# Performance work log

Measured on AMD Instinct MI355X. Metric: run time of the kernel, lower is better.

The kernel has to match this reference:

```python
import jax, jax.numpy as jnp
import numpy as np

B, S, E = 8, 4096, 512
QKV, H = 512, 8
D = QKV // H  # head_dim = 64
EPS = 1e-6


def setup_inputs() -> dict:
    key = jax.random.key(0)
    ks = jax.random.split(key, 9)
    sc_in = 1.0 / np.sqrt(E)
    sc_qkv = 1.0 / np.sqrt(QKV)
    # Linear weights stored as [in, out] so y = x @ W + b (equivalent to torch x @ W_t.T + b)
    return {
        "x": jax.random.normal(ks[0], (B, S, E), dtype=jnp.float32),
        "Wq": jax.random.uniform(ks[1], (E, QKV), jnp.float32, -sc_in, sc_in),
        "bq": jax.random.uniform(ks[2], (QKV,), jnp.float32, -sc_in, sc_in),
        "Wk": jax.random.uniform(ks[3], (E, QKV), jnp.float32, -sc_in, sc_in),
        "bk": jax.random.uniform(ks[4], (QKV,), jnp.float32, -sc_in, sc_in),
        "Wv": jax.random.uniform(ks[5], (E, QKV), jnp.float32, -sc_in, sc_in),
        "bv": jax.random.uniform(ks[6], (QKV,), jnp.float32, -sc_in, sc_in),
        "Wo": jax.random.uniform(ks[7], (QKV, E), jnp.float32, -sc_qkv, sc_qkv),
        "bo": jax.random.uniform(ks[8], (E,), jnp.float32, -sc_qkv, sc_qkv),
    }


def feature_map(t):
    # elu(x) + 1 (always positive features)
    return jax.nn.elu(t) + 1.0


def reference(x, Wq, bq, Wk, bk, Wv, bv, Wo, bo):
    bs, seqlen, _ = x.shape
    q = (x @ Wq + bq).reshape(bs, seqlen, H, D)
    k = (x @ Wk + bk).reshape(bs, seqlen, H, D)
    v = (x @ Wv + bv).reshape(bs, seqlen, H, D)
    q = feature_map(q)
    k = feature_map(k)
    # kv: [n, h, m, d] -- per-head outer-product accumulation over sequence
    kv = jnp.einsum('nshd,nshm->nhmd', k, v)
    # normalizer z: [n, l, h]
    z = 1.0 / (jnp.einsum('nlhd,nhd->nlh', q, k.sum(axis=1)) + EPS)
    out = jnp.einsum('nlhd,nhmd,nlh->nlhm', q, kv, z)
    out = out.reshape(bs, seqlen, QKV)
    return out @ Wo + bo
```

## Files before the change

kernel.cpp:

```cpp
#include <hip/hip_runtime.h>
#include <hip/hip_bf16.h>


typedef __bf16 bf16x8 __attribute__((ext_vector_type(8)));
typedef float  f32x4  __attribute__((ext_vector_type(4)));

__device__ __forceinline__ float b2f(unsigned short u) {
    unsigned int x = ((unsigned int)u) << 16;
    return __builtin_bit_cast(float, x);
}
__device__ __forceinline__ unsigned short f2b(float f) {
    unsigned int u = __builtin_bit_cast(unsigned int, f);
    unsigned int r = (u + 0x7FFFu + ((u >> 16) & 1u)) >> 16;
    return (unsigned short)r;
}
__device__ __forceinline__ void load_lds16(const unsigned short* g, unsigned short* l) {
    __builtin_amdgcn_global_load_lds(
        (const __attribute__((address_space(1))) void*)g,
        (__attribute__((address_space(3))) void*)l, 16, 0, 0);
}

__global__ void prep_kernel(const float* __restrict__ x,
                            const float* __restrict__ w0, const float* __restrict__ w1,
                            const float* __restrict__ w2, const float* __restrict__ w3,
                            unsigned short* __restrict__ xb, unsigned short* __restrict__ wt,
                            float* __restrict__ ksg) {
    __shared__ float tile[64][65];
    int t = threadIdx.x;
    if (blockIdx.x >= 256) {
        int i = (blockIdx.x - 256) * 256 + t;
        float4 v = ((const float4*)x)[i];
        ushort4 o;
        o.x = f2b(v.x); o.y = f2b(v.y); o.z = f2b(v.z); o.w = f2b(v.w);
        ((ushort4*)xb)[i] = o;
        return;
    }
    int idx = blockIdx.x;
    if (idx < 16) ksg[idx * 256 + t] = 0.f;
    int bz = idx >> 6, by = (idx >> 3) & 7, bx = idx & 7;
    const float* src = (bz == 0) ? w0 : (bz == 1) ? w1 : (bz == 2) ? w2 : w3;
    unsigned short* dst = wt + (size_t)bz * 512 * 512;
    int rb = by * 64, cb = bx * 64;
    #pragma unroll
    for (int i = 0; i < 16; i++) {
        int c = t + i * 256; int r = c >> 6, cc = c & 63;
        tile[r][cc] = src[(rb + r) * 512 + cb + cc];
    }
    __syncthreads();
    #pragma unroll
    for (int i = 0; i < 16; i++) {
        int c = t + i * 256; int r = c >> 6, cc = c & 63;
        dst[(cb + r) * 512 + rb + cc] = f2b(tile[cc][r]);
    }
}

__global__ __launch_bounds__(256, 4) void gemm_qkv_kernel(
        const unsigned short* __restrict__ xb, const unsigned short* __restrict__ wt,
        const float* __restrict__ bq, const float* __restrict__ bk, const float* __restrict__ bv,
        unsigned short* __restrict__ qb, unsigned short* __restrict__ kT,
        unsigned short* __restrict__ vT, float* __restrict__ ksg) {
    int g = blockIdx.x;
    int xcd = g & 7, slot = g >> 3;
    int mtile = xcd * 32 + slot / 12;
    int tn = slot % 12;
    int tensor = tn >> 2, ntile = tn & 3;
    const unsigned short* Bt = wt + (size_t)tensor * 512 * 512;
    const float* bias = tensor == 0 ? bq : tensor == 1 ? bk : bv;
    bool act = tensor < 2;

    __shared__ __align__(16) unsigned short sA[128 * 64];
    __shared__ __align__(16) unsigned short sB[128 * 64];
    const int tid  = threadIdx.x;
    const int wave = tid >> 6, lane = tid & 63;
    const int wm = wave >> 1, wn = wave & 1;
    const int quad = lane >> 4, l16 = lane & 15;
    const int mbase = mtile * 128, nbase = ntile * 128;
    const int rsub = lane >> 3;
    const int coff = (((lane & 7) ^ rsub) << 3);

    f32x4 acc[4][4];
    #pragma unroll
    for (int i = 0; i < 4; i++)
        #pragma unroll
        for (int j = 0; j < 4; j++) acc[i][j] = (f32x4){0.f, 0.f, 0.f, 0.f};

    for (int kb = 0; kb < 512; kb += 64) {
        #pragma unroll
        for (int t = 0; t < 4; t++) {
            int r0 = t * 32 + wave * 8;
            load_lds16(&xb[(size_t)(mbase + r0 + rsub) * 512 + kb + coff], &sA[r0 * 64]);
            load_lds16(&Bt[(size_t)(nbase + r0 + rsub) * 512 + kb + coff], &sB[r0 * 64]);
        }
        __syncthreads();
        #pragma unroll
        for (int ko = 0; ko < 64; ko += 32) {
            bf16x8 af[4], bfr[4];
            int pg = ((quad + (ko >> 3)) ^ (l16 & 7)) << 3;
            #pragma unroll
            for (int f = 0; f < 4; f++)
                af[f] = *(const bf16x8*)&sA[(wm * 64 + f * 16 + l16) * 64 + pg];
            #pragma unroll
            for (int f = 0; f < 4; f++)
                bfr[f] = *(const bf16x8*)&sB[(wn * 64 + f * 16 + l16) * 64 + pg];
            #pragma unroll
            for (int i = 0; i < 4; i++)
                #pragma unroll
                for (int j = 0; j < 4; j++)
                    acc[i][j] = __builtin_amdgcn_mfma_f32_16x16x32_bf16(af[i], bfr[j], acc[i][j], 0, 0, 0);
        }
        __syncthreads();
    }
    if (tensor == 0) {
        #pragma unroll
        for (int i = 0; i < 4; i++)
            #pragma unroll
            for (int j = 0; j < 4; j++) {
                int gcol = nbase + wn * 64 + j * 16 + l16;
                float bv = bias[gcol];
                #pragma unroll
                for (int r = 0; r < 4; r++) {
                    int grow = mbase + wm * 64 + i * 16 + quad * 4 + r;
                    float v = acc[i][j][r] + bv;
                    v = v > 0.f ? v + 1.f : __expf(v);
                    qb[(size_t)grow * 512 + gcol] = f2b(v);
                }
            }
    } else {
        unsigned short* T = (tensor == 1) ? kT : vT;
        float csum[4] = {0.f, 0.f, 0.f, 0.f};
        #pragma unroll
        for (int i = 0; i < 4; i++)
            #pragma unroll
            for (int j = 0; j < 4; j++) {
                int gcol = nbase + wn * 64 + j * 16 + l16;
                int h = gcol >> 6, d = gcol & 63;
                float bv = bias[gcol];
                int grow0 = mbase + wm * 64 + i * 16 + quad * 4;
                int b = grow0 >> 12, s0 = grow0 & 4095;
                ushort4 o;
                #pragma unroll
                for (int r = 0; r < 4; r++) {
                    float v = acc[i][j][r] + bv;
                    if (act) { v = v > 0.f ? v + 1.f : __expf(v); csum[j] += v; }
                    ((unsigned short*)&o)[r] = f2b(v);
                }
                *(ushort4*)&T[(((size_t)b * 8 + h) * 64 + d) * 4096 + s0] = o;
            }
        if (act) {
            int b = mbase >> 12;
            #pragma unroll
            for (int j = 0; j < 4; j++) {
                float s = csum[j];
                s += __shfl_xor(s, 16, 64);
                s += __shfl_xor(s, 32, 64);
                if (quad == 0) {
                    int gcol = nbase + wn * 64 + j * 16 + l16;
                    atomicAdd(&ksg[b * 512 + gcol], s);
                }
            }
        }
    }
}

__global__ __launch_bounds__(256, 4) void kv_kernel(
        const unsigned short* __restrict__ kT, const unsigned short* __restrict__ vT,
        float* __restrict__ kvp) {
    int bh = blockIdx.x >> 4, sc = blockIdx.x & 15;
    const int tid = threadIdx.x;
    const int wave = tid >> 6, lane = tid & 63;
    const int wm = wave >> 1, wn = wave & 1;
    const int quad = lane >> 4, l16 = lane & 15;
    const int rsub = lane >> 3;
    const int coff = (((lane & 7) ^ rsub) << 3);
    __shared__ __align__(16) unsigned short sV[64 * 64];
    __shared__ __align__(16) unsigned short sK[64 * 64];

    f32x4 acc[2][2];
    #pragma unroll
    for (int i = 0; i < 2; i++)
        #pragma unroll
        for (int j = 0; j < 2; j++) acc[i][j] = (f32x4){0.f, 0.f, 0.f, 0.f};
    size_t base = (size_t)bh * 64 * 4096 + sc * 256;

    for (int kb = 0; kb < 4; kb++) {
        int s0 = kb * 64;
        #pragma unroll
        for (int t = 0; t < 2; t++) {
            int r0 = t * 32 + wave * 8;
            load_lds16(&vT[base + (size_t)(r0 + rsub) * 4096 + s0 + coff], &sV[r0 * 64]);
            load_lds16(&kT[base + (size_t)(r0 + rsub) * 4096 + s0 + coff], &sK[r0 * 64]);
        }
        __syncthreads();
        #pragma unroll
        for (int ko = 0; ko < 64; ko += 32) {
            bf16x8 af[2], bfr[2];
            int pg = ((quad + (ko >> 3)) ^ (l16 & 7)) << 3;
            #pragma unroll
            for (int f = 0; f < 2; f++)
                af[f] = *(const bf16x8*)&sV[(wm * 32 + f * 16 + l16) * 64 + pg];
            #pragma unroll
            for (int f = 0; f < 2; f++)
                bfr[f] = *(const bf16x8*)&sK[(wn * 32 + f * 16 + l16) * 64 + pg];
            #pragma unroll
            for (int i = 0; i < 2; i++)
                #pragma unroll
                for (int j = 0; j < 2; j++)
                    acc[i][j] = __builtin_amdgcn_mfma_f32_16x16x32_bf16(af[i], bfr[j], acc[i][j], 0, 0, 0);
        }
        __syncthreads();
    }
    float* kvout = kvp + ((size_t)sc * 64 + bh) * 4096;
    #pragma unroll
    for (int i = 0; i < 2; i++)
        #pragma unroll
        for (int j = 0; j < 2; j++)
            #pragma unroll
            for (int r = 0; r < 4; r++) {
                int m = wm * 32 + i * 16 + quad * 4 + r;
                int d = wn * 32 + j * 16 + l16;
                kvout[m * 64 + d] = acc[i][j][r];
            }
}

__global__ __launch_bounds__(256) void mid_kernel(
        const float* __restrict__ kvp, unsigned short* __restrict__ kvb) {
    int bh = blockIdx.x >> 2, part = blockIdx.x & 3;
    int tid = threadIdx.x;
    int idx = (part * 256 + tid) * 4;
    float s0 = 0.f, s1 = 0.f, s2 = 0.f, s3 = 0.f;
    #pragma unroll
    for (int sc = 0; sc < 16; sc++) {
        float4 v = *(const float4*)&kvp[((size_t)sc * 64 + bh) * 4096 + idx];
        s0 += v.x; s1 += v.y; s2 += v.z; s3 += v.w;
    }
    ushort4 o; o.x = f2b(s0); o.y = f2b(s1); o.z = f2b(s2); o.w = f2b(s3);
    *(ushort4*)&kvb[(size_t)bh * 4096 + idx] = o;
}

__global__ __launch_bounds__(256, 2) void fused_out_kernel(
        const unsigned short* __restrict__ qb,
        const unsigned short* __restrict__ kvb, const float* __restrict__ ksg,
        const unsigned short* __restrict__ wto, const float* __restrict__ bo,
        float* __restrict__ out) {
    int g = blockIdx.x;
    int xcd = g & 7, slot = g >> 3;
    int mtile = xcd * 32 + (slot >> 2);
    int ntile = slot & 3;

    __shared__ __align__(16) unsigned short sQ[128 * 64];
    __shared__ __align__(16) unsigned short sWo[128 * 64];
    __shared__ __align__(16) unsigned short sKV[64 * 64];
    __shared__ __align__(16) unsigned short sO1[128 * 64];
    __shared__ float sKsum[512];
    __shared__ float sZ[128];
    const int tid  = threadIdx.x;
    const int wave = tid >> 6, lane = tid & 63;
    const int wm = wave >> 1, wn = wave & 1;
    const int quad = lane >> 4, l16 = lane & 15;
    const int mbase = mtile * 128, nbase = ntile * 128;
    const int b = mtile >> 5;
    const int rsub = lane >> 3;
    const int coff = (((lane & 7) ^ rsub) << 3);

    sKsum[tid]       = ksg[b * 512 + tid];
    sKsum[tid + 256] = ksg[b * 512 + 256 + tid];

    f32x4 accm[4][4];
    #pragma unroll
    for (int i = 0; i < 4; i++)
        #pragma unroll
        for (int j = 0; j < 4; j++) accm[i][j] = (f32x4){0.f, 0.f, 0.f, 0.f};

    for (int h = 0; h < 8; h++) {
        #pragma unroll
        for (int t = 0; t < 4; t++) {
            int r0 = t * 32 + wave * 8;
            load_lds16(&qb[(size_t)(mbase + r0 + rsub) * 512 + h * 64 + coff], &sQ[r0 * 64]);
            load_lds16(&wto[(size_t)(nbase + r0 + rsub) * 512 + h * 64 + coff], &sWo[r0 * 64]);
        }
        #pragma unroll
        for (int t = 0; t < 2; t++) {
            int r0 = t * 32 + wave * 8;
            load_lds16(&kvb[(size_t)(b * 8 + h) * 4096 + (r0 + rsub) * 64 + coff], &sKV[r0 * 64]);
        }
        __syncthreads();
        {
            int row = tid >> 1, half = tid & 1;
            const float* ksh = &sKsum[h * 64];
            float dsum = 0.f;
            #pragma unroll
            for (int g2 = 0; g2 < 4; g2++) {
                int G = half * 4 + g2;
                uint4 w = *(const uint4*)&sQ[row * 64 + ((G ^ (row & 7)) << 3)];
                const unsigned int* qp = (const unsigned int*)&w;
                #pragma unroll
                for (int u = 0; u < 4; u++) {
                    int c = G * 8 + u * 2;
                    dsum += __builtin_bit_cast(float, qp[u] << 16)        * ksh[c];
                    dsum += __builtin_bit_cast(float, qp[u] & 0xFFFF0000u) * ksh[c + 1];
                }
            }
            dsum += __shfl_xor(dsum, 1, 64);
            if (!half) sZ[row] = 1.f / (dsum + 1e-6f);
        }
        __syncthreads();
        f32x4 acco[4][2];
        #pragma unroll
        for (int f = 0; f < 4; f++)
            #pragma unroll
            for (int j = 0; j < 2; j++) acco[f][j] = (f32x4){0.f, 0.f, 0.f, 0.f};
        #pragma unroll
        for (int ko = 0; ko < 64; ko += 32) {
            bf16x8 af[4], bfr[2];
            int pg = ((quad + (ko >> 3)) ^ (l16 & 7)) << 3;
            #pragma unroll
            for (int f = 0; f < 4; f++)
                af[f] = *(const bf16x8*)&sQ[(wm * 64 + f * 16 + l16) * 64 + pg];
            #pragma unroll
            for (int j = 0; j < 2; j++)
                bfr[j] = *(const bf16x8*)&sKV[(wn * 32 + j * 16 + l16) * 64 + pg];
            #pragma unroll
            for (int f = 0; f < 4; f++)
                #pragma unroll
                for (int j = 0; j < 2; j++)
                    acco[f][j] = __builtin_amdgcn_mfma_f32_16x16x32_bf16(af[f], bfr[j], acco[f][j], 0, 0, 0);
        }
        #pragma unroll
        for (int f = 0; f < 4; f++)
            #pragma unroll
            for (int j = 0; j < 2; j++)
                #pragma unroll
                for (int r = 0; r < 4; r++) {
                    int row = wm * 64 + f * 16 + quad * 4 + r;
                    int col = wn * 32 + j * 16 + l16;
                    float v = acco[f][j][r] * sZ[row];
                    int grp = col >> 3;
                    sO1[row * 64 + ((grp ^ (row & 7)) << 3) + (col & 7)] = f2b(v);
                }
        __syncthreads();
        #pragma unroll
        for (int ko = 0; ko < 64; ko += 32) {
            bf16x8 af[4], bfr[4];
            int pg = ((quad + (ko >> 3)) ^ (l16 & 7)) << 3;
            #pragma unroll
            for (int f = 0; f < 4; f++)
                af[f] = *(const bf16x8*)&sO1[(wm * 64 + f * 16 + l16) * 64 + pg];
            #pragma unroll
            for (int f = 0; f < 4; f++)
                bfr[f] = *(const bf16x8*)&sWo[(wn * 64 + f * 16 + l16) * 64 + pg];
            #pragma unroll
            for (int i = 0; i < 4; i++)
                #pragma unroll
                for (int j = 0; j < 4; j++)
                    accm[i][j] = __builtin_amdgcn_mfma_f32_16x16x32_bf16(af[i], bfr[j], accm[i][j], 0, 0, 0);
        }
        __syncthreads();
    }
    #pragma unroll
    for (int i = 0; i < 4; i++)
        #pragma unroll
        for (int j = 0; j < 4; j++) {
            int gcol = nbase + wn * 64 + j * 16 + l16;
            float bv = bo[gcol];
            #pragma unroll
            for (int r = 0; r < 4; r++) {
                int grow = mbase + wm * 64 + i * 16 + quad * 4 + r;
                out[(size_t)grow * 512 + gcol] = accm[i][j][r] + bv;
            }
        }
}

extern "C" void kernel_launch(void* const* d_in, const int* in_sizes, int n_in,
                              void* d_out, int out_size, void* d_ws, size_t ws_size,
                              hipStream_t stream) {
    const float* x  = (const float*)d_in[0];
    const float* Wq = (const float*)d_in[1];
    const float* bq = (const float*)d_in[2];
    const float* Wk = (const float*)d_in[3];
    const float* bk = (const float*)d_in[4];
    const float* Wv = (const float*)d_in[5];
    const float* bv = (const float*)d_in[6];
    const float* Wo = (const float*)d_in[7];
    const float* bo = (const float*)d_in[8];
    float* out = (float*)d_out;

    char* wsb = (char*)d_ws;
    char* ob  = (char*)d_out;
    unsigned short* vT  = (unsigned short*)ob;
    unsigned short* xb  = (unsigned short*)(ob + 33554432ull);
    float*          kvp = (float*)(ob + 33554432ull);
    unsigned short* qb  = (unsigned short*)wsb;
    unsigned short* kT  = (unsigned short*)(wsb + 33554432ull);
    unsigned short* wt  = (unsigned short*)(wsb + 67108864ull);
    unsigned short* kvb = (unsigned short*)(wsb + 69206016ull);
    float*          ksg = (float*)(wsb + 69730304ull);

    prep_kernel<<<16640, 256, 0, stream>>>(x, Wq, Wk, Wv, Wo, xb, wt, ksg);
    gemm_qkv_kernel<<<3072, 256, 0, stream>>>(xb, wt, bq, bk, bv, qb, kT, vT, ksg);
    kv_kernel<<<1024, 256, 0, stream>>>(kT, vT, kvp);
    mid_kernel<<<256, 256, 0, stream>>>(kvp, kvb);
    fused_out_kernel<<<1024, 256, 0, stream>>>(qb, kvb, ksg,
            wt + 3ull * 512 * 512, bo, out);
}
```

Before: 259.8 us.

## Widen output tiles to 256 columns and halve kv sequence splits

The fused output kernel now computes a 128x256 output tile per block, two Wo tiles per head. This halves the redundant per-block recomputation of the attention numerator (q·kv and normalizer) and the repeated Q/KV loads. The kv kernel splits the sequence into 8 chunks instead of 16, which halves the partial-sum traffic reduced in mid_kernel. In exchange, doubled accumulators and extra LDS raise register pressure and may reduce occupancy, and the grids shrink to 512 blocks.

Result: faster. 242.5 us (-6.7%).

```diff
diff --git a/kernel.cpp b/kernel.cpp
--- a/kernel.cpp
+++ b/kernel.cpp
@@ -165,7 +165,7 @@
 __global__ __launch_bounds__(256, 4) void kv_kernel(
         const unsigned short* __restrict__ kT, const unsigned short* __restrict__ vT,
         float* __restrict__ kvp) {
-    int bh = blockIdx.x >> 4, sc = blockIdx.x & 15;
+    int bh = blockIdx.x >> 3, sc = blockIdx.x & 7;
     const int tid = threadIdx.x;
     const int wave = tid >> 6, lane = tid & 63;
     const int wm = wave >> 1, wn = wave & 1;
@@ -180,9 +180,9 @@
     for (int i = 0; i < 2; i++)
         #pragma unroll
         for (int j = 0; j < 2; j++) acc[i][j] = (f32x4){0.f, 0.f, 0.f, 0.f};
-    size_t base = (size_t)bh * 64 * 4096 + sc * 256;
-
-    for (int kb = 0; kb < 4; kb++) {
+    size_t base = (size_t)bh * 64 * 4096 + sc * 512;
+
+    for (int kb = 0; kb < 8; kb++) {
         int s0 = kb * 64;
         #pragma unroll
         for (int t = 0; t < 2; t++) {
@@ -229,7 +229,7 @@
     int idx = (part * 256 + tid) * 4;
     float s0 = 0.f, s1 = 0.f, s2 = 0.f, s3 = 0.f;
     #pragma unroll
-    for (int sc = 0; sc < 16; sc++) {
+    for (int sc = 0; sc < 8; sc++) {
         float4 v = *(const float4*)&kvp[((size_t)sc * 64 + bh) * 4096 + idx];
         s0 += v.x; s1 += v.y; s2 += v.z; s3 += v.w;
     }
@@ -244,11 +244,11 @@
         float* __restrict__ out) {
     int g = blockIdx.x;
     int xcd = g & 7, slot = g >> 3;
-    int mtile = xcd * 32 + (slot >> 2);
-    int ntile = slot & 3;
+    int mtile = xcd * 32 + (slot >> 1);
+    int np = slot & 1;
 
     __shared__ __align__(16) unsigned short sQ[128 * 64];
-    __shared__ __align__(16) unsigned short sWo[128 * 64];
+    __shared__ __align__(16) unsigned short sWo[2][128 * 64];
     __shared__ __align__(16) unsigned short sKV[64 * 64];
     __shared__ __align__(16) unsigned short sO1[128 * 64];
     __shared__ float sKsum[512];
@@ -257,7 +257,7 @@
     const int wave = tid >> 6, lane = tid & 63;
     const int wm = wave >> 1, wn = wave & 1;
     const int quad = lane >> 4, l16 = lane & 15;
-    const int mbase = mtile * 128, nbase = ntile * 128;
+    const int mbase = mtile * 128, nbase = np * 256;
     const int b = mtile >> 5;
     const int rsub = lane >> 3;
     const int coff = (((lane & 7) ^ rsub) << 3);
@@ -265,18 +265,21 @@
     sKsum[tid]       = ksg[b * 512 + tid];
     sKsum[tid + 256] = ksg[b * 512 + 256 + tid];
 
-    f32x4 accm[4][4];
-    #pragma unroll
-    for (int i = 0; i < 4; i++)
-        #pragma unroll
-        for (int j = 0; j < 4; j++) accm[i][j] = (f32x4){0.f, 0.f, 0.f, 0.f};
+    f32x4 accm[2][4][4];
+    #pragma unroll
+    for (int n = 0; n < 2; n++)
+        #pragma unroll
+        for (int i = 0; i < 4; i++)
+            #pragma unroll
+            for (int j = 0; j < 4; j++) accm[n][i][j] = (f32x4){0.f, 0.f, 0.f, 0.f};
 
     for (int h = 0; h < 8; h++) {
         #pragma unroll
         for (int t = 0; t < 4; t++) {
             int r0 = t * 32 + wave * 8;
             load_lds16(&qb[(size_t)(mbase + r0 + rsub) * 512 + h * 64 + coff], &sQ[r0 * 64]);
-            load_lds16(&wto[(size_t)(nbase + r0 + rsub) * 512 + h * 64 + coff], &sWo[r0 * 64]);
+            load_lds16(&wto[(size_t)(nbase + r0 + rsub) * 512 + h * 64 + coff], &sWo[0][r0 * 64]);
+            load_lds16(&wto[(size_t)(nbase + 128 + r0 + rsub) * 512 + h * 64 + coff], &sWo[1][r0 * 64]);
         }
         #pragma unroll
         for (int t = 0; t < 2; t++) {
@@ -340,34 +343,40 @@
         __syncthreads();
         #pragma unroll
         for (int ko = 0; ko < 64; ko += 32) {
-            bf16x8 af[4], bfr[4];
+            bf16x8 af[4], bfr0[4], bfr1[4];
             int pg = ((quad + (ko >> 3)) ^ (l16 & 7)) << 3;
             #pragma unroll
             for (int f = 0; f < 4; f++)
                 af[f] = *(const bf16x8*)&sO1[(wm * 64 + f * 16 + l16) * 64 + pg];
             #pragma unroll
-            for (int f = 0; f < 4; f++)
-                bfr[f] = *(const bf16x8*)&sWo[(wn * 64 + f * 16 + l16) * 64 + pg];
+            for (int f = 0; f < 4; f++) {
+                bfr0[f] = *(const bf16x8*)&sWo[0][(wn * 64 + f * 16 + l16) * 64 + pg];
+                bfr1[f] = *(const bf16x8*)&sWo[1][(wn * 64 + f * 16 + l16) * 64 + pg];
+            }
             #pragma unroll
             for (int i = 0; i < 4; i++)
                 #pragma unroll
-                for (int j = 0; j < 4; j++)
-                    accm[i][j] = __builtin_amdgcn_mfma_f32_16x16x32_bf16(af[i], bfr[j], accm[i][j], 0, 0, 0);
-        }
-        __syncthreads();
-    }
-    #pragma unroll
-    for (int i = 0; i < 4; i++)
-        #pragma unroll
-        for (int j = 0; j < 4; j++) {
-            int gcol = nbase + wn * 64 + j * 16 + l16;
-            float bv = bo[gcol];
-            #pragma unroll
-            for (int r = 0; r < 4; r++) {
-                int grow = mbase + wm * 64 + i * 16 + quad * 4 + r;
-                out[(size_t)grow * 512 + gcol] = accm[i][j][r] + bv;
-            }
-        }
+                for (int j = 0; j < 4; j++) {
+                    accm[0][i][j] = __builtin_amdgcn_mfma_f32_16x16x32_bf16(af[i], bfr0[j], accm[0][i][j], 0, 0, 0);
+                    accm[1][i][j] = __builtin_amdgcn_mfma_f32_16x16x32_bf16(af[i], bfr1[j], accm[1][i][j], 0, 0, 0);
+                }
+        }
+        __syncthreads();
+    }
+    #pragma unroll
+    for (int n = 0; n < 2; n++)
+        #pragma unroll
+        for (int i = 0; i < 4; i++)
+            #pragma unroll
+            for (int j = 0; j < 4; j++) {
+                int gcol = nbase + n * 128 + wn * 64 + j * 16 + l16;
+                float bv = bo[gcol];
+                #pragma unroll
+                for (int r = 0; r < 4; r++) {
+                    int grow = mbase + wm * 64 + i * 16 + quad * 4 + r;
+                    out[(size_t)grow * 512 + gcol] = accm[n][i][j][r] + bv;
+                }
+            }
 }
 
 extern "C" void kernel_launch(void* const* d_in, const int* in_sizes, int n_in,
@@ -397,8 +406,8 @@
 
     prep_kernel<<<16640, 256, 0, stream>>>(x, Wq, Wk, Wv, Wo, xb, wt, ksg);
     gemm_qkv_kernel<<<3072, 256, 0, stream>>>(xb, wt, bq, bk, bv, qb, kT, vT, ksg);
-    kv_kernel<<<1024, 256, 0, stream>>>(kT, vT, kvp);
+    kv_kernel<<<512, 256, 0, stream>>>(kT, vT, kvp);
     mid_kernel<<<256, 256, 0, stream>>>(kvp, kvb);
-    fused_out_kernel<<<1024, 256, 0, stream>>>(qb, kvb, ksg,
+    fused_out_kernel<<<512, 256, 0, stream>>>(qb, kvb, ksg,
             wt + 3ull * 512 * 512, bo, out);
 }
```
